# Performance work log

Measured on AMD Instinct MI355X. Metric: run time of the kernel, lower is better.

The kernel has to match this reference:

```python
import jax, jax.numpy as jnp
import numpy as np

H = 1024
E = 8
K = 2
N = 16384
LN_EPS = 1e-5


def _layernorm(h, g, b):
    m = jnp.mean(h, axis=-1, keepdims=True)
    v = jnp.mean(jnp.square(h - m), axis=-1, keepdims=True)
    return (h - m) * jax.lax.rsqrt(v + LN_EPS) * g + b


def setup_inputs() -> dict:
    key = jax.random.key(0)
    ks = jax.random.split(key, 8)
    s = 0.02
    return {
        "x": jax.random.normal(ks[0], (N, H), dtype=jnp.float32),
        "Wg": jax.random.normal(ks[1], (H, E), dtype=jnp.float32) * s,
        "bg": jnp.zeros((E,), dtype=jnp.float32),
        "W1": jax.random.normal(ks[2], (E, H, H), dtype=jnp.float32) * s,
        "b1": jnp.zeros((E, H), dtype=jnp.float32),
        "g1": jnp.ones((E, H), dtype=jnp.float32),
        "be1": jnp.zeros((E, H), dtype=jnp.float32),
        "W2": jax.random.normal(ks[3], (E, H, H), dtype=jnp.float32) * s,
        "b2": jnp.zeros((E, H), dtype=jnp.float32),
        "g2": jnp.ones((E, H), dtype=jnp.float32),
        "be2": jnp.zeros((E, H), dtype=jnp.float32),
    }


def reference(x, Wg, bg, W1, b1, g1, be1, W2, b2, g2, be2):
    # Gating: softmax over experts, top-k, renormalize
    gate_probs = jax.nn.softmax(x @ Wg + bg, axis=1)            # [N, E]
    tk_p, tk_i = jax.lax.top_k(gate_probs, K)                    # [N, K]
    tk_p = tk_p / (jnp.sum(tk_p, axis=1, keepdims=True) + 1e-9)
    # Dense per-expert combine weight (zero where expert not selected)
    w = jnp.sum(tk_p[:, :, None] * jax.nn.one_hot(tk_i, E, dtype=x.dtype), axis=1)  # [N, E]

    # ResidualBlock per expert, computed densely for all tokens (dropout = eval/no-op)
    h = jnp.einsum('nh,eho->eno', x, W1) + b1[:, None, :]        # [E, N, H]
    h = jax.nn.relu(_layernorm(h, g1[:, None, :], be1[:, None, :]))
    h = jnp.einsum('enh,eho->eno', h, W2) + b2[:, None, :]
    h = _layernorm(h, g2[:, None, :], be2[:, None, :])
    y = jax.nn.relu(x[None, :, :] + h)                           # [E, N, H]

    moe_out = jnp.einsum('ne,enh->nh', w, y)                     # [N, H]
    return moe_out, gate_probs
```

## Files before the change

### kernel.cpp

```cpp
#include <hip/hip_runtime.h>
#include <cstdint>
#include <cstddef>

constexpr int H_DIM = 1024;
constexpr int NE    = 8;
constexpr int NT    = 16384;
constexpr int NP    = NT * 2;

typedef __attribute__((ext_vector_type(8))) short          short8;
typedef __attribute__((ext_vector_type(8))) unsigned short ushort8;
typedef __attribute__((ext_vector_type(4))) unsigned short ushort4v;
typedef __attribute__((ext_vector_type(4))) float          f32x4;

__device__ __forceinline__ unsigned short f2bf(float f) {
  union { float f; uint32_t u; } c; c.f = f;
  uint32_t u = c.u;
  u = (u + 0x7fffu + ((u >> 16) & 1u)) >> 16;
  return (unsigned short)u;
}
__device__ __forceinline__ float bf2f(unsigned short h) {
  union { uint32_t u; float f; } c; c.u = ((uint32_t)h) << 16;
  return c.f;
}

__device__ __forceinline__ void gload16(const unsigned short* g, unsigned short* l) {
  __builtin_amdgcn_global_load_lds((const __attribute__((address_space(1))) void*)g,
                                   (__attribute__((address_space(3))) void*)l, 16, 0, 0);
}

__global__ __launch_bounds__(256) void transpose_convert_kernel(
    const float* __restrict__ W1, const float* __restrict__ W2,
    unsigned short* __restrict__ T1, unsigned short* __restrict__ T2)
{
  __shared__ float tile[64][65];
  int zi = blockIdx.z;
  const float* W = (zi < 8) ? W1 : W2;
  unsigned short* T = (zi < 8) ? T1 : T2;
  int e  = zi & 7;
  int o0 = blockIdx.x * 64;
  int h0 = blockIdx.y * 64;
  int c  = threadIdx.x & 63;
  int r0 = (threadIdx.x >> 6) * 16;
  const float* src = W + ((size_t)e * H_DIM + h0) * H_DIM + o0;
#pragma unroll
  for (int i = 0; i < 16; ++i)
    tile[r0 + i][c] = src[(size_t)(r0 + i) * H_DIM + c];
  __syncthreads();
  unsigned short* dst = T + ((size_t)e * H_DIM + o0) * H_DIM + h0;
#pragma unroll
  for (int i = 0; i < 16; ++i)
    dst[(size_t)(r0 + i) * H_DIM + c] = f2bf(tile[c][r0 + i]);
}

__global__ __launch_bounds__(256) void xgate_kernel(
    const float* __restrict__ X, const float* __restrict__ Wg,
    const float* __restrict__ bg, unsigned short* __restrict__ Xb,
    float* __restrict__ gate_out, int* __restrict__ tk_e, float* __restrict__ tk_w)
{
  int wid = threadIdx.x >> 6, lane = threadIdx.x & 63;
  int n = blockIdx.x * 4 + wid;
  const float* xr = X + (size_t)n * H_DIM;

  const float4* xp = (const float4*)(xr + lane * 16);
  float4 f0 = xp[0], f1 = xp[1], f2 = xp[2], f3 = xp[3];
  float v[16] = {f0.x,f0.y,f0.z,f0.w, f1.x,f1.y,f1.z,f1.w,
                 f2.x,f2.y,f2.z,f2.w, f3.x,f3.y,f3.z,f3.w};

  ushort8 u0, u1;
#pragma unroll
  for (int j = 0; j < 8; ++j) { u0[j] = f2bf(v[j]); u1[j] = f2bf(v[8 + j]); }
  ushort8* xb = (ushort8*)(Xb + (size_t)n * H_DIM + lane * 16);
  xb[0] = u0; xb[1] = u1;

  float acc[8];
#pragma unroll
  for (int e = 0; e < 8; ++e) acc[e] = 0.f;
#pragma unroll
  for (int j = 0; j < 16; ++j) {
    int h = lane * 16 + j;
    const float4* wg = (const float4*)(Wg + (size_t)h * 8);
    float4 a = wg[0], b = wg[1];
    float xv = v[j];
    acc[0] += xv * a.x; acc[1] += xv * a.y; acc[2] += xv * a.z; acc[3] += xv * a.w;
    acc[4] += xv * b.x; acc[5] += xv * b.y; acc[6] += xv * b.z; acc[7] += xv * b.w;
  }
#pragma unroll
  for (int m = 1; m < 64; m <<= 1) {
#pragma unroll
    for (int e = 0; e < 8; ++e) acc[e] += __shfl_xor(acc[e], m);
  }
#pragma unroll
  for (int e = 0; e < 8; ++e) acc[e] += bg[e];

  float mx = acc[0];
#pragma unroll
  for (int e = 1; e < 8; ++e) mx = fmaxf(mx, acc[e]);
  float g[8], s = 0.f;
#pragma unroll
  for (int e = 0; e < 8; ++e) { g[e] = __expf(acc[e] - mx); s += g[e]; }
  float inv = 1.f / s;
#pragma unroll
  for (int e = 0; e < 8; ++e) g[e] *= inv;

  int e0 = 0; float b0 = g[0];
#pragma unroll
  for (int e = 1; e < 8; ++e) if (g[e] > b0) { b0 = g[e]; e0 = e; }
  int e1 = -1; float b1v = -1.f;
#pragma unroll
  for (int e = 0; e < 8; ++e) if (e != e0 && g[e] > b1v) { b1v = g[e]; e1 = e; }
  float s2 = b0 + b1v + 1e-9f;

  if (lane == 0) {
    float4* gp = (float4*)(gate_out + (size_t)n * 8);
    gp[0] = make_float4(g[0], g[1], g[2], g[3]);
    gp[1] = make_float4(g[4], g[5], g[6], g[7]);
    tk_e[2 * n] = e0; tk_e[2 * n + 1] = e1;
    tk_w[2 * n] = b0 / s2; tk_w[2 * n + 1] = b1v / s2;
  }
}

__global__ __launch_bounds__(256) void hist_kernel(
    const int* __restrict__ tk_e, int* __restrict__ blockHist)
{
  __shared__ int h[8];
  if (threadIdx.x < 8) h[threadIdx.x] = 0;
  __syncthreads();
  int i0 = blockIdx.x * 512 + threadIdx.x;
  atomicAdd(&h[tk_e[i0]], 1);
  atomicAdd(&h[tk_e[i0 + 256]], 1);
  __syncthreads();
  if (threadIdx.x < 8) blockHist[blockIdx.x * 8 + threadIdx.x] = h[threadIdx.x];
}

__global__ void scan_kernel(const int* __restrict__ blockHist,
                            int* __restrict__ blockBase,
                            int* __restrict__ count, int* __restrict__ offs)
{
  int e = threadIdx.x;
  if (e < 8) {
    int run = 0;
    for (int b = 0; b < 64; ++b) { blockBase[b * 8 + e] = run; run += blockHist[b * 8 + e]; }
    count[e] = run;
  }
  __syncthreads();
  if (threadIdx.x == 0) {
    int o = 0;
    for (int k = 0; k < 8; ++k) { offs[k] = o; o += count[k]; }
  }
  __syncthreads();
  if (e < 8) {
    int o = offs[e];
    for (int b = 0; b < 64; ++b) blockBase[b * 8 + e] += o;
  }
}

__global__ __launch_bounds__(256) void place_kernel(
    const int* __restrict__ tk_e, const int* __restrict__ blockBase,
    int* __restrict__ pairTok, int* __restrict__ pairExp, int* __restrict__ slots)
{
  __shared__ int cur[8];
  if (threadIdx.x < 8) cur[threadIdx.x] = blockBase[blockIdx.x * 8 + threadIdx.x];
  __syncthreads();
#pragma unroll
  for (int j = 0; j < 2; ++j) {
    int i = blockIdx.x * 512 + j * 256 + threadIdx.x;
    int e = tk_e[i];
    int s = atomicAdd(&cur[e], 1);
    pairTok[s] = i >> 1; pairExp[s] = e; slots[i] = s;
  }
}

template<bool GATHER>
__global__ __launch_bounds__(256) void gemm_kernel(
    const unsigned short* __restrict__ Ab,
    const unsigned short* __restrict__ Bt,
    const float* __restrict__ bias,
    const int* __restrict__ pairTok,
    const int* __restrict__ count, const int* __restrict__ offs,
    unsigned short* __restrict__ Out)
{
  __shared__ unsigned short As[128 * 32];
  __shared__ unsigned short Bs[128 * 32];

  const int e  = blockIdx.z;
  const int mt = blockIdx.y;
  const int nt = blockIdx.x;
  const int cnt = count[e];
  if (mt * 128 >= cnt) return;
  const int base = offs[e];
  const int tid = threadIdx.x;
  const int w = tid >> 6, l = tid & 63;

  const int r0 = w * 16 + (l >> 2);
  const int kk = (l & 3) * 8;

  int m0 = mt * 128 + r0;      if (m0 >= cnt) m0 = cnt - 1;
  int m1 = mt * 128 + r0 + 64; if (m1 >= cnt) m1 = cnt - 1;
  size_t arow0, arow1;
  if (GATHER) { arow0 = (size_t)pairTok[base + m0]; arow1 = (size_t)pairTok[base + m1]; }
  else        { arow0 = (size_t)(base + m0);        arow1 = (size_t)(base + m1); }
  const unsigned short* aS0 = Ab + arow0 * H_DIM + kk;
  const unsigned short* aS1 = Ab + arow1 * H_DIM + kk;
  const unsigned short* bS0 = Bt + ((size_t)e * H_DIM + nt * 128 + r0) * H_DIM + kk;
  const unsigned short* bS1 = bS0 + (size_t)64 * H_DIM;
  unsigned short* aD0 = As + w * 512;
  unsigned short* aD1 = As + 2048 + w * 512;
  unsigned short* bD0 = Bs + w * 512;
  unsigned short* bD1 = Bs + 2048 + w * 512;

  const int wr = w >> 1, wc = w & 1;
  const int lr = l & 15, lg = l >> 4;

  f32x4 acc[4][4] = {};

  for (int k0 = 0; k0 < H_DIM; k0 += 32) {
    __syncthreads();
    gload16(aS0 + k0, aD0);
    gload16(aS1 + k0, aD1);
    gload16(bS0 + k0, bD0);
    gload16(bS1 + k0, bD1);
    __syncthreads();

    short8 af[4], bfr[4];
#pragma unroll
    for (int i = 0; i < 4; ++i) {
      af[i]  = *(const short8*)&As[(wr * 64 + i * 16 + lr) * 32 + lg * 8];
      bfr[i] = *(const short8*)&Bs[(wc * 64 + i * 16 + lr) * 32 + lg * 8];
    }
#pragma unroll
    for (int m4 = 0; m4 < 4; ++m4)
#pragma unroll
      for (int n4 = 0; n4 < 4; ++n4)
        acc[m4][n4] = __builtin_amdgcn_mfma_f32_16x16x32_bf16(af[m4], bfr[n4], acc[m4][n4], 0, 0, 0);
  }

#pragma unroll
  for (int n4 = 0; n4 < 4; ++n4) {
    int col = nt * 128 + wc * 64 + n4 * 16 + lr;
    float bv = bias[e * H_DIM + col];
#pragma unroll
    for (int m4 = 0; m4 < 4; ++m4) {
#pragma unroll
      for (int r = 0; r < 4; ++r) {
        int grow = mt * 128 + wr * 64 + m4 * 16 + 4 * lg + r;
        if (grow < cnt)
          Out[(size_t)(base + grow) * H_DIM + col] = f2bf(acc[m4][n4][r] + bv);
      }
    }
  }
}

__global__ __launch_bounds__(256) void ln_relu_kernel(
    unsigned short* __restrict__ buf, const float* __restrict__ gamma,
    const float* __restrict__ beta, const int* __restrict__ pairExp)
{
  int wid = threadIdx.x >> 6, lane = threadIdx.x & 63;
  int row = blockIdx.x * 4 + wid;
  int e = pairExp[row];
  unsigned short* r = buf + (size_t)row * H_DIM;
  ushort8 u0 = ((const ushort8*)r)[lane];
  ushort8 u1 = ((const ushort8*)r)[lane + 64];
  float v[16];
#pragma unroll
  for (int j = 0; j < 8; ++j) { v[j] = bf2f(u0[j]); v[8 + j] = bf2f(u1[j]); }
  float s = 0.f, ss = 0.f;
#pragma unroll
  for (int j = 0; j < 16; ++j) { s += v[j]; ss += v[j] * v[j]; }
#pragma unroll
  for (int m = 1; m < 64; m <<= 1) { s += __shfl_xor(s, m); ss += __shfl_xor(ss, m); }
  float mean = s * (1.f / 1024.f);
  float var  = ss * (1.f / 1024.f) - mean * mean;
  float rs   = rsqrtf(var + 1e-5f);

  int h0 = lane * 8, h1 = 512 + lane * 8;
  const float4* gp0 = (const float4*)(gamma + (size_t)e * H_DIM + h0);
  const float4* bp0 = (const float4*)(beta  + (size_t)e * H_DIM + h0);
  const float4* gp1 = (const float4*)(gamma + (size_t)e * H_DIM + h1);
  const float4* bp1 = (const float4*)(beta  + (size_t)e * H_DIM + h1);
  float4 ga = gp0[0], gb = gp0[1], gc = gp1[0], gd = gp1[1];
  float4 ba = bp0[0], bb = bp0[1], bc = bp1[0], bd = bp1[1];
  float gv[16] = {ga.x,ga.y,ga.z,ga.w, gb.x,gb.y,gb.z,gb.w,
                  gc.x,gc.y,gc.z,gc.w, gd.x,gd.y,gd.z,gd.w};
  float bv[16] = {ba.x,ba.y,ba.z,ba.w, bb.x,bb.y,bb.z,bb.w,
                  bc.x,bc.y,bc.z,bc.w, bd.x,bd.y,bd.z,bd.w};
#pragma unroll
  for (int j = 0; j < 8; ++j) {
    float t0 = fmaxf((v[j]     - mean) * rs * gv[j]     + bv[j],     0.f);
    float t1 = fmaxf((v[8 + j] - mean) * rs * gv[8 + j] + bv[8 + j], 0.f);
    u0[j] = f2bf(t0); u1[j] = f2bf(t1);
  }
  ((ushort8*)r)[lane] = u0; ((ushort8*)r)[lane + 64] = u1;
}

__global__ __launch_bounds__(256) void combine_kernel(
    const unsigned short* __restrict__ buf2, const float* __restrict__ X,
    const float* __restrict__ g2, const float* __restrict__ be2,
    const int* __restrict__ slots, const int* __restrict__ tk_e,
    const float* __restrict__ tk_w, float* __restrict__ out)
{
  int wid = threadIdx.x >> 6, lane = threadIdx.x & 63;
  int n = blockIdx.x * 4 + wid;
  int h0 = lane * 8, h1 = 512 + lane * 8;

  const float4* xp0 = (const float4*)(X + (size_t)n * H_DIM + h0);
  const float4* xp1 = (const float4*)(X + (size_t)n * H_DIM + h1);
  float4 xa = xp0[0], xb = xp0[1], xc = xp1[0], xd = xp1[1];
  float xv[16] = {xa.x,xa.y,xa.z,xa.w, xb.x,xb.y,xb.z,xb.w,
                  xc.x,xc.y,xc.z,xc.w, xd.x,xd.y,xd.z,xd.w};
  float o[16];
#pragma unroll
  for (int j = 0; j < 16; ++j) o[j] = 0.f;

#pragma unroll
  for (int k = 0; k < 2; ++k) {
    int slot = slots[2 * n + k];
    int e = tk_e[2 * n + k];
    float w = tk_w[2 * n + k];
    const unsigned short* r = buf2 + (size_t)slot * H_DIM;
    ushort8 u0 = ((const ushort8*)r)[lane];
    ushort8 u1 = ((const ushort8*)r)[lane + 64];
    float v[16];
#pragma unroll
    for (int j = 0; j < 8; ++j) { v[j] = bf2f(u0[j]); v[8 + j] = bf2f(u1[j]); }
    float s = 0.f, ss = 0.f;
#pragma unroll
    for (int j = 0; j < 16; ++j) { s += v[j]; ss += v[j] * v[j]; }
#pragma unroll
    for (int m = 1; m < 64; m <<= 1) { s += __shfl_xor(s, m); ss += __shfl_xor(ss, m); }
    float mean = s * (1.f / 1024.f);
    float var  = ss * (1.f / 1024.f) - mean * mean;
    float rs   = rsqrtf(var + 1e-5f);

    const float4* gp0 = (const float4*)(g2  + (size_t)e * H_DIM + h0);
    const float4* bp0 = (const float4*)(be2 + (size_t)e * H_DIM + h0);
    const float4* gp1 = (const float4*)(g2  + (size_t)e * H_DIM + h1);
    const float4* bp1 = (const float4*)(be2 + (size_t)e * H_DIM + h1);
    float4 ga = gp0[0], gb = gp0[1], gc = gp1[0], gd = gp1[1];
    float4 ba = bp0[0], bb = bp0[1], bc = bp1[0], bd = bp1[1];
    float gv[16] = {ga.x,ga.y,ga.z,ga.w, gb.x,gb.y,gb.z,gb.w,
                    gc.x,gc.y,gc.z,gc.w, gd.x,gd.y,gd.z,gd.w};
    float bvv[16] = {ba.x,ba.y,ba.z,ba.w, bb.x,bb.y,bb.z,bb.w,
                     bc.x,bc.y,bc.z,bc.w, bd.x,bd.y,bd.z,bd.w};
#pragma unroll
    for (int j = 0; j < 16; ++j) {
      float u = (v[j] - mean) * rs * gv[j] + bvv[j];
      float y = fmaxf(xv[j] + u, 0.f);
      o[j] += w * y;
    }
  }

  float4* op0 = (float4*)(out + (size_t)n * H_DIM + h0);
  float4* op1 = (float4*)(out + (size_t)n * H_DIM + h1);
  op0[0] = make_float4(o[0], o[1], o[2], o[3]);
  op0[1] = make_float4(o[4], o[5], o[6], o[7]);
  op1[0] = make_float4(o[8], o[9], o[10], o[11]);
  op1[1] = make_float4(o[12], o[13], o[14], o[15]);
}

extern "C" void kernel_launch(void* const* d_in, const int* in_sizes, int n_in,
                              void* d_out, int out_size, void* d_ws, size_t ws_size,
                              hipStream_t stream)
{
  const float* x   = (const float*)d_in[0];
  const float* Wg  = (const float*)d_in[1];
  const float* bg  = (const float*)d_in[2];
  const float* W1  = (const float*)d_in[3];
  const float* b1  = (const float*)d_in[4];
  const float* g1  = (const float*)d_in[5];
  const float* be1 = (const float*)d_in[6];
  const float* W2  = (const float*)d_in[7];
  const float* b2  = (const float*)d_in[8];
  const float* g2  = (const float*)d_in[9];
  const float* be2 = (const float*)d_in[10];
  float* out = (float*)d_out;
  float* gate_out = out + (size_t)NT * H_DIM;

  char* ws = (char*)d_ws;
  size_t off = 0;
  auto alloc = [&](size_t bytes) { char* p = ws + off; off += (bytes + 255) & ~(size_t)255; return p; };
  unsigned short* w1bt = (unsigned short*)alloc((size_t)NE * H_DIM * H_DIM * 2);
  unsigned short* w2bt = (unsigned short*)alloc((size_t)NE * H_DIM * H_DIM * 2);
  unsigned short* buf1 = (unsigned short*)alloc((size_t)NP * H_DIM * 2);
  unsigned short* buf2 = (unsigned short*)alloc((size_t)NP * H_DIM * 2);
  int*   tk_e      = (int*)alloc((size_t)NP * 4);
  float* tk_w      = (float*)alloc((size_t)NP * 4);
  int*   pairTok   = (int*)alloc((size_t)NP * 4);
  int*   pairExp   = (int*)alloc((size_t)NP * 4);
  int*   slots     = (int*)alloc((size_t)NP * 4);
  int*   blockHist = (int*)alloc(64 * 8 * 4);
  int*   blockBase = (int*)alloc(64 * 8 * 4);
  int*   count     = (int*)alloc(8 * 4);
  int*   offs      = (int*)alloc(8 * 4);
  (void)in_sizes; (void)n_in; (void)out_size; (void)ws_size;

  unsigned short* Xb = buf2;

  transpose_convert_kernel<<<dim3(16, 16, 16), 256, 0, stream>>>(W1, W2, w1bt, w2bt);
  xgate_kernel<<<dim3(NT / 4), 256, 0, stream>>>(x, Wg, bg, Xb, gate_out, tk_e, tk_w);
  hist_kernel<<<dim3(64), 256, 0, stream>>>(tk_e, blockHist);
  scan_kernel<<<dim3(1), 64, 0, stream>>>(blockHist, blockBase, count, offs);
  place_kernel<<<dim3(64), 256, 0, stream>>>(tk_e, blockBase, pairTok, pairExp, slots);
  gemm_kernel<true><<<dim3(8, 128, 8), 256, 0, stream>>>(
      Xb, w1bt, b1, pairTok, count, offs, buf1);
  ln_relu_kernel<<<dim3(NP / 4), 256, 0, stream>>>(buf1, g1, be1, pairExp);
  gemm_kernel<false><<<dim3(8, 128, 8), 256, 0, stream>>>(
      buf1, w2bt, b2, pairTok, count, offs, buf2);
  combine_kernel<<<dim3(NT / 4), 256, 0, stream>>>(
      buf2, x, g2, be2, slots, tk_e, tk_w, out);
}
```

Measured before the change: 423.9 us.

## Rewrite grouped expert GEMM with 256x256 tiles, double-buffering, and compact worklist

The grouped expert GEMM moves from 128x128x32 tiles with 4 waves to 256x256x64 tiles with 8 waves. LDS is double-buffered with an XOR swizzle, and the next tiles are prefetched asynchronously while MFMAs run, with raised priority around the MFMA block. A new worklist kernel builds a compact list of the non-empty (expert, n-tile, m-tile) tiles, and blocks are remapped across the XCDs so empty tiles are not launched and neighbouring tiles share cache. The aim is more data reuse per load, overlap of load latency with compute, and less launch waste, at the cost of larger LDS and register use plus one extra tiny kernel.

```diff
diff --git a/kernel.cpp b/kernel.cpp
--- a/kernel.cpp
+++ b/kernel.cpp
@@ -7,9 +7,12 @@
 constexpr int NT    = 16384;
 constexpr int NP    = NT * 2;
 
+constexpr int BM = 256, BN = 256, BK = 64;
+constexpr int NKT = H_DIM / BK;
+constexpr int MAX_WG = NE * (NT / BM) * (H_DIM / BN);
+
 typedef __attribute__((ext_vector_type(8))) short          short8;
 typedef __attribute__((ext_vector_type(8))) unsigned short ushort8;
-typedef __attribute__((ext_vector_type(4))) unsigned short ushort4v;
 typedef __attribute__((ext_vector_type(4))) float          f32x4;
 
 __device__ __forceinline__ unsigned short f2bf(float f) {
@@ -170,84 +173,182 @@
   }
 }
 
+__global__ void worklist_kernel(const int* __restrict__ count,
+                                int* __restrict__ wl, int* __restrict__ wlCount)
+{
+  __shared__ int nmt[8], ebase[8], totalS;
+  if (threadIdx.x == 0) {
+    int o = 0;
+    for (int e = 0; e < 8; ++e) {
+      nmt[e] = (count[e] + BM - 1) / BM;
+      ebase[e] = o;
+      o += nmt[e] * (H_DIM / BN);
+    }
+    totalS = o;
+    wlCount[0] = o;
+  }
+  __syncthreads();
+  int total = totalS;
+  for (int i = threadIdx.x; i < total; i += blockDim.x) {
+    int e = 0;
+    while (e < 7 && i >= ebase[e + 1]) ++e;
+    int loc = i - ebase[e];
+    int nt = loc / nmt[e];
+    int mt = loc - nt * nmt[e];
+    wl[i] = (e << 20) | (nt << 16) | mt;
+  }
+}
+
 template<bool GATHER>
-__global__ __launch_bounds__(256) void gemm_kernel(
+__global__ __launch_bounds__(512, 2) void gemm8_kernel(
     const unsigned short* __restrict__ Ab,
     const unsigned short* __restrict__ Bt,
     const float* __restrict__ bias,
     const int* __restrict__ pairTok,
     const int* __restrict__ count, const int* __restrict__ offs,
+    const int* __restrict__ wl, const int* __restrict__ wlCount,
     unsigned short* __restrict__ Out)
 {
-  __shared__ unsigned short As[128 * 32];
-  __shared__ unsigned short Bs[128 * 32];
-
-  const int e  = blockIdx.z;
-  const int mt = blockIdx.y;
-  const int nt = blockIdx.x;
-  const int cnt = count[e];
-  if (mt * 128 >= cnt) return;
-  const int base = offs[e];
+  __shared__ unsigned short As[2 * 2 * 8192];
+  __shared__ unsigned short Bs[2 * 2 * 8192];
+
+  const int total = wlCount[0];
+  const int orig = blockIdx.x;
+  if (orig >= total) return;
+  const int qq = total >> 3, rr = total & 7;
+  const int xcd = orig & 7, sub = orig >> 3;
+  const int idx = (xcd < rr ? xcd * (qq + 1) : rr * (qq + 1) + (xcd - rr) * qq) + sub;
+  const int ent = wl[idx];
+  const int e = ent >> 20, ntb = (ent >> 16) & 15, mtb = ent & 0xffff;
+  const int cnt = count[e], base = offs[e];
+
   const int tid = threadIdx.x;
-  const int w = tid >> 6, l = tid & 63;
-
-  const int r0 = w * 16 + (l >> 2);
-  const int kk = (l & 3) * 8;
-
-  int m0 = mt * 128 + r0;      if (m0 >= cnt) m0 = cnt - 1;
-  int m1 = mt * 128 + r0 + 64; if (m1 >= cnt) m1 = cnt - 1;
-  size_t arow0, arow1;
-  if (GATHER) { arow0 = (size_t)pairTok[base + m0]; arow1 = (size_t)pairTok[base + m1]; }
-  else        { arow0 = (size_t)(base + m0);        arow1 = (size_t)(base + m1); }
-  const unsigned short* aS0 = Ab + arow0 * H_DIM + kk;
-  const unsigned short* aS1 = Ab + arow1 * H_DIM + kk;
-  const unsigned short* bS0 = Bt + ((size_t)e * H_DIM + nt * 128 + r0) * H_DIM + kk;
-  const unsigned short* bS1 = bS0 + (size_t)64 * H_DIM;
-  unsigned short* aD0 = As + w * 512;
-  unsigned short* aD1 = As + 2048 + w * 512;
-  unsigned short* bD0 = Bs + w * 512;
-  unsigned short* bD1 = Bs + 2048 + w * 512;
-
-  const int wr = w >> 1, wc = w & 1;
-  const int lr = l & 15, lg = l >> 4;
-
-  f32x4 acc[4][4] = {};
-
-  for (int k0 = 0; k0 < H_DIM; k0 += 32) {
-    __syncthreads();
-    gload16(aS0 + k0, aD0);
-    gload16(aS1 + k0, aD1);
-    gload16(bS0 + k0, bD0);
-    gload16(bS1 + k0, bD1);
-    __syncthreads();
-
-    short8 af[4], bfr[4];
-#pragma unroll
-    for (int i = 0; i < 4; ++i) {
-      af[i]  = *(const short8*)&As[(wr * 64 + i * 16 + lr) * 32 + lg * 8];
-      bfr[i] = *(const short8*)&Bs[(wc * 64 + i * 16 + lr) * 32 + lg * 8];
+  const int wid = tid >> 6, l = tid & 63;
+  const int wr = wid >> 2, wc = wid & 3;
+
+  const int rih0 = (((tid >> 6)) >> 1) * 16 + ((tid >> 2) & 15);
+  const int rih1 = ((8 + (tid >> 6)) >> 1) * 16 + ((tid >> 2) & 15);
+  const int selem = ((tid >> 6) & 1) * 32 + (((tid & 3) * 8) ^ (((tid >> 5) & 1) << 4));
+
+  const unsigned short* ap[4];
+  const unsigned short* bp[4];
+  {
+    int g0 = mtb * 256 + rih0;       if (g0 >= cnt) g0 = cnt - 1;
+    int g1 = mtb * 256 + rih1;       if (g1 >= cnt) g1 = cnt - 1;
+    int g2 = mtb * 256 + 128 + rih0; if (g2 >= cnt) g2 = cnt - 1;
+    int g3 = mtb * 256 + 128 + rih1; if (g3 >= cnt) g3 = cnt - 1;
+    size_t r0, r1, r2, r3;
+    if (GATHER) {
+      r0 = (size_t)pairTok[base + g0]; r1 = (size_t)pairTok[base + g1];
+      r2 = (size_t)pairTok[base + g2]; r3 = (size_t)pairTok[base + g3];
+    } else {
+      r0 = (size_t)(base + g0); r1 = (size_t)(base + g1);
+      r2 = (size_t)(base + g2); r3 = (size_t)(base + g3);
     }
-#pragma unroll
-    for (int m4 = 0; m4 < 4; ++m4)
-#pragma unroll
-      for (int n4 = 0; n4 < 4; ++n4)
-        acc[m4][n4] = __builtin_amdgcn_mfma_f32_16x16x32_bf16(af[m4], bfr[n4], acc[m4][n4], 0, 0, 0);
-  }
-
-#pragma unroll
-  for (int n4 = 0; n4 < 4; ++n4) {
-    int col = nt * 128 + wc * 64 + n4 * 16 + lr;
-    float bv = bias[e * H_DIM + col];
-#pragma unroll
-    for (int m4 = 0; m4 < 4; ++m4) {
-#pragma unroll
-      for (int r = 0; r < 4; ++r) {
-        int grow = mt * 128 + wr * 64 + m4 * 16 + 4 * lg + r;
-        if (grow < cnt)
-          Out[(size_t)(base + grow) * H_DIM + col] = f2bf(acc[m4][n4][r] + bv);
-      }
+    ap[0] = Ab + r0 * H_DIM + selem;
+    ap[1] = Ab + r1 * H_DIM + selem;
+    ap[2] = Ab + r2 * H_DIM + selem;
+    ap[3] = Ab + r3 * H_DIM + selem;
+    const unsigned short* bbase = Bt + ((size_t)e * H_DIM + ntb * 256) * H_DIM + selem;
+    bp[0] = bbase + (size_t)(rih0)       * H_DIM;
+    bp[1] = bbase + (size_t)(rih1)       * H_DIM;
+    bp[2] = bbase + (size_t)(128 + rih0) * H_DIM;
+    bp[3] = bbase + (size_t)(128 + rih1) * H_DIM;
+  }
+
+#define A_DST(t, h, i) (As + ((t) & 1) * 16384 + (h) * 8192 + (i) * 4096 + wid * 512)
+#define B_DST(t, h, i) (Bs + ((t) & 1) * 16384 + (h) * 8192 + (i) * 4096 + wid * 512)
+
+  const int loff = ((l & 15) * 64 + (l >> 4) * 16) ^ (((l >> 3) & 1) << 5);
+  const char* AsB = (const char*)As + wr * 16384 + loff;
+  const char* BsB = (const char*)Bs + (wc >> 1) * 16384 + loff;
+  const int bsub = (wc & 1) * 4;
+
+  gload16(ap[0], A_DST(0, 0, 0)); gload16(ap[1], A_DST(0, 0, 1));
+  gload16(ap[2], A_DST(0, 1, 0)); gload16(ap[3], A_DST(0, 1, 1));
+  gload16(bp[0], B_DST(0, 0, 0)); gload16(bp[1], B_DST(0, 0, 1));
+  gload16(bp[2], B_DST(0, 1, 0)); gload16(bp[3], B_DST(0, 1, 1));
+  gload16(bp[0] + BK, B_DST(1, 0, 0)); gload16(bp[1] + BK, B_DST(1, 0, 1));
+  gload16(bp[2] + BK, B_DST(1, 1, 0)); gload16(bp[3] + BK, B_DST(1, 1, 1));
+  asm volatile("s_waitcnt vmcnt(4)" ::: "memory");
+  __builtin_amdgcn_s_barrier();
+
+  f32x4 acc[8][4] = {};
+
+  for (int t = 0; t < NKT; ++t) {
+    const int db = t & 1;
+    const int dboff = db * 32768;
+    short8 bfrag[4][2];
+#pragma unroll
+    for (int q = 0; q < 4; ++q) {
+      short8 af[2][2];
+#pragma unroll
+      for (int j = 0; j < 2; ++j)
+#pragma unroll
+        for (int ks = 0; ks < 2; ++ks)
+          af[j][ks] = *(const short8*)(AsB + dboff + ((q * 2 + j) * 2 + ks) * 1024);
+      if (q == 0) {
+#pragma unroll
+        for (int r = 0; r < 4; ++r)
+#pragma unroll
+          for (int ks = 0; ks < 2; ++ks)
+            bfrag[r][ks] = *(const short8*)(BsB + dboff + ((bsub + r) * 2 + ks) * 1024);
+      }
+      if (q == 0 && t + 1 < NKT) {
+        gload16(ap[0] + (t + 1) * BK, A_DST(t + 1, 0, 0));
+        gload16(ap[1] + (t + 1) * BK, A_DST(t + 1, 0, 1));
+      }
+      if (q == 1 && t + 1 < NKT) {
+        gload16(ap[2] + (t + 1) * BK, A_DST(t + 1, 1, 0));
+        gload16(ap[3] + (t + 1) * BK, A_DST(t + 1, 1, 1));
+      }
+      if (q == 2 && t + 2 < NKT) {
+        gload16(bp[0] + (t + 2) * BK, B_DST(t + 2, 0, 0));
+        gload16(bp[1] + (t + 2) * BK, B_DST(t + 2, 0, 1));
+      }
+      if (q == 3 && t + 2 < NKT) {
+        gload16(bp[2] + (t + 2) * BK, B_DST(t + 2, 1, 0));
+        gload16(bp[3] + (t + 2) * BK, B_DST(t + 2, 1, 1));
+      }
+      __builtin_amdgcn_s_barrier();
+      __builtin_amdgcn_s_setprio(1);
+#pragma unroll
+      for (int j = 0; j < 2; ++j)
+#pragma unroll
+        for (int r = 0; r < 4; ++r)
+#pragma unroll
+          for (int ks = 0; ks < 2; ++ks)
+            acc[q * 2 + j][r] = __builtin_amdgcn_mfma_f32_16x16x32_bf16(
+                af[j][ks], bfrag[r][ks], acc[q * 2 + j][r], 0, 0, 0);
+      __builtin_amdgcn_s_setprio(0);
+      if (q == 3) {
+        if (t + 2 < NKT) asm volatile("s_waitcnt vmcnt(4)" ::: "memory");
+        else             asm volatile("s_waitcnt vmcnt(0)" ::: "memory");
+      }
+      __builtin_amdgcn_s_barrier();
     }
   }
+
+  float bvv[4];
+#pragma unroll
+  for (int r = 0; r < 4; ++r)
+    bvv[r] = bias[e * H_DIM + ntb * 256 + wc * 64 + r * 16 + (l & 15)];
+#pragma unroll
+  for (int j = 0; j < 8; ++j) {
+    int grow0 = mtb * 256 + wr * 128 + j * 16 + (l >> 4) * 4;
+#pragma unroll
+    for (int r = 0; r < 4; ++r) {
+      int gcol = ntb * 256 + wc * 64 + r * 16 + (l & 15);
+#pragma unroll
+      for (int v = 0; v < 4; ++v) {
+        int row = grow0 + v;
+        if (row < cnt)
+          Out[(size_t)(base + row) * H_DIM + gcol] = f2bf(acc[j][r][v] + bvv[r]);
+      }
+    }
+  }
+#undef A_DST
+#undef B_DST
 }
 
 __global__ __launch_bounds__(256) void ln_relu_kernel(
@@ -391,6 +492,8 @@
   int*   blockBase = (int*)alloc(64 * 8 * 4);
   int*   count     = (int*)alloc(8 * 4);
   int*   offs      = (int*)alloc(8 * 4);
+  int*   wl        = (int*)alloc(MAX_WG * 4);
+  int*   wlCount   = (int*)alloc(4);
   (void)in_sizes; (void)n_in; (void)out_size; (void)ws_size;
 
   unsigned short* Xb = buf2;
@@ -399,12 +502,13 @@
   xgate_kernel<<<dim3(NT / 4), 256, 0, stream>>>(x, Wg, bg, Xb, gate_out, tk_e, tk_w);
   hist_kernel<<<dim3(64), 256, 0, stream>>>(tk_e, blockHist);
   scan_kernel<<<dim3(1), 64, 0, stream>>>(blockHist, blockBase, count, offs);
+  worklist_kernel<<<dim3(1), 256, 0, stream>>>(count, wl, wlCount);
   place_kernel<<<dim3(64), 256, 0, stream>>>(tk_e, blockBase, pairTok, pairExp, slots);
-  gemm_kernel<true><<<dim3(8, 128, 8), 256, 0, stream>>>(
-      Xb, w1bt, b1, pairTok, count, offs, buf1);
+  gemm8_kernel<true><<<dim3(MAX_WG), 512, 0, stream>>>(
+      Xb, w1bt, b1, pairTok, count, offs, wl, wlCount, buf1);
   ln_relu_kernel<<<dim3(NP / 4), 256, 0, stream>>>(buf1, g1, be1, pairExp);
-  gemm_kernel<false><<<dim3(8, 128, 8), 256, 0, stream>>>(
-      buf1, w2bt, b2, pairTok, count, offs, buf2);
+  gemm8_kernel<false><<<dim3(MAX_WG), 512, 0, stream>>>(
+      buf1, w2bt, b2, pairTok, count, offs, wl, wlCount, buf2);
   combine_kernel<<<dim3(NT / 4), 256, 0, stream>>>(
       buf2, x, g2, be2, slots, tk_e, tk_w, out);
 }
```

Result: faster. 413.4 us (-2.5%).

## Replace expert GEMM with 256x256 double-buffered 8-phase pipelined kernel over compact worklist

Applied to the files above, without the earlier changes.

Swaps the 128x128, K=32 single-buffered expert GEMM for a 512-thread kernel that computes 256x256 tiles with K=64. It double-buffers swizzled LDS tiles and interleaves global-to-LDS loads with MFMA phases, using explicit barriers, waitcnts and setprio. The scan kernel now also builds a compact worklist of the non-empty expert tiles, and the work-item index is remapped so consecutive items land on the same XCD. The aim is more data reuse per byte loaded, hidden memory latency and fewer idle blocks. In exchange it uses 128KB of LDS per block, which limits occupancy to one block per CU, and the hand-written synchronisation is fragile.

```diff
diff --git a/kernel.cpp b/kernel.cpp
--- a/kernel.cpp
+++ b/kernel.cpp
@@ -7,9 +7,12 @@
 constexpr int NT    = 16384;
 constexpr int NP    = NT * 2;
 
+constexpr int GBM = 256, GBN = 256, GBK = 64;
+constexpr int GNKT = H_DIM / GBK;
+constexpr int MAX_WG = (NP / GBM + NE) * (H_DIM / GBN);
+
 typedef __attribute__((ext_vector_type(8))) short          short8;
 typedef __attribute__((ext_vector_type(8))) unsigned short ushort8;
-typedef __attribute__((ext_vector_type(4))) unsigned short ushort4v;
 typedef __attribute__((ext_vector_type(4))) float          f32x4;
 
 __device__ __forceinline__ unsigned short f2bf(float f) {
@@ -132,10 +135,12 @@
   if (threadIdx.x < 8) blockHist[blockIdx.x * 8 + threadIdx.x] = h[threadIdx.x];
 }
 
-__global__ void scan_kernel(const int* __restrict__ blockHist,
-                            int* __restrict__ blockBase,
-                            int* __restrict__ count, int* __restrict__ offs)
-{
+__global__ void scan_worklist_kernel(const int* __restrict__ blockHist,
+                                     int* __restrict__ blockBase,
+                                     int* __restrict__ count, int* __restrict__ offs,
+                                     int* __restrict__ wl, int* __restrict__ wlCount)
+{
+  __shared__ int nmt[8], ebase[8], totalS;
   int e = threadIdx.x;
   if (e < 8) {
     int run = 0;
@@ -144,13 +149,27 @@
   }
   __syncthreads();
   if (threadIdx.x == 0) {
-    int o = 0;
-    for (int k = 0; k < 8; ++k) { offs[k] = o; o += count[k]; }
+    int o = 0, wo = 0;
+    for (int k = 0; k < 8; ++k) {
+      offs[k] = o; o += count[k];
+      nmt[k] = (count[k] + GBM - 1) / GBM;
+      ebase[k] = wo; wo += nmt[k] * (H_DIM / GBN);
+    }
+    totalS = wo; wlCount[0] = wo;
   }
   __syncthreads();
   if (e < 8) {
     int o = offs[e];
     for (int b = 0; b < 64; ++b) blockBase[b * 8 + e] += o;
+  }
+  int total = totalS;
+  for (int i = threadIdx.x; i < total; i += blockDim.x) {
+    int ee = 0;
+    while (ee < 7 && i >= ebase[ee + 1]) ++ee;
+    int loc = i - ebase[ee];
+    int nt = loc / nmt[ee];
+    int mt = loc - nt * nmt[ee];
+    wl[i] = (ee << 20) | (nt << 16) | mt;
   }
 }
 
@@ -171,83 +190,161 @@
 }
 
 template<bool GATHER>
-__global__ __launch_bounds__(256) void gemm_kernel(
+__global__ __launch_bounds__(512, 2) void gemm8p_kernel(
     const unsigned short* __restrict__ Ab,
     const unsigned short* __restrict__ Bt,
     const float* __restrict__ bias,
     const int* __restrict__ pairTok,
     const int* __restrict__ count, const int* __restrict__ offs,
+    const int* __restrict__ wl, const int* __restrict__ wlCount,
     unsigned short* __restrict__ Out)
 {
-  __shared__ unsigned short As[128 * 32];
-  __shared__ unsigned short Bs[128 * 32];
-
-  const int e  = blockIdx.z;
-  const int mt = blockIdx.y;
-  const int nt = blockIdx.x;
-  const int cnt = count[e];
-  if (mt * 128 >= cnt) return;
-  const int base = offs[e];
+  __shared__ unsigned short lds[65536];
+
+  const int total = wlCount[0];
+  const int orig = blockIdx.x;
+  if (orig >= total) return;
+  const int qq = total >> 3, rr = total & 7;
+  const int xcd = orig & 7, sub = orig >> 3;
+  const int idx = (xcd < rr ? xcd * (qq + 1) : rr * (qq + 1) + (xcd - rr) * qq) + sub;
+  const int ent = wl[idx];
+  const int e = ent >> 20, ntb = (ent >> 16) & 15, mtb = ent & 0xffff;
+  const int cnt = count[e], base = offs[e];
+
   const int tid = threadIdx.x;
-  const int w = tid >> 6, l = tid & 63;
-
-  const int r0 = w * 16 + (l >> 2);
-  const int kk = (l & 3) * 8;
-
-  int m0 = mt * 128 + r0;      if (m0 >= cnt) m0 = cnt - 1;
-  int m1 = mt * 128 + r0 + 64; if (m1 >= cnt) m1 = cnt - 1;
-  size_t arow0, arow1;
-  if (GATHER) { arow0 = (size_t)pairTok[base + m0]; arow1 = (size_t)pairTok[base + m1]; }
-  else        { arow0 = (size_t)(base + m0);        arow1 = (size_t)(base + m1); }
-  const unsigned short* aS0 = Ab + arow0 * H_DIM + kk;
-  const unsigned short* aS1 = Ab + arow1 * H_DIM + kk;
-  const unsigned short* bS0 = Bt + ((size_t)e * H_DIM + nt * 128 + r0) * H_DIM + kk;
-  const unsigned short* bS1 = bS0 + (size_t)64 * H_DIM;
-  unsigned short* aD0 = As + w * 512;
-  unsigned short* aD1 = As + 2048 + w * 512;
-  unsigned short* bD0 = Bs + w * 512;
-  unsigned short* bD1 = Bs + 2048 + w * 512;
-
-  const int wr = w >> 1, wc = w & 1;
-  const int lr = l & 15, lg = l >> 4;
-
-  f32x4 acc[4][4] = {};
-
-  for (int k0 = 0; k0 < H_DIM; k0 += 32) {
-    __syncthreads();
-    gload16(aS0 + k0, aD0);
-    gload16(aS1 + k0, aD1);
-    gload16(bS0 + k0, bD0);
-    gload16(bS1 + k0, bD1);
-    __syncthreads();
-
-    short8 af[4], bfr[4];
-#pragma unroll
-    for (int i = 0; i < 4; ++i) {
-      af[i]  = *(const short8*)&As[(wr * 64 + i * 16 + lr) * 32 + lg * 8];
-      bfr[i] = *(const short8*)&Bs[(wc * 64 + i * 16 + lr) * 32 + lg * 8];
+  const int wid = tid >> 6, l = tid & 63;
+  const int wr = wid >> 2, wc = wid & 3;
+
+  const int rwh  = (wid >> 1) * 16 + (l >> 2);
+  const int ksl  = wid & 1;
+  const int koff = ksl * 32 + (((l & 3) * 8) ^ (((l >> 5) & 1) << 4));
+
+  const unsigned short* aptr[2][2];
+  const unsigned short* bptr[2][2];
+#pragma unroll
+  for (int ha = 0; ha < 2; ++ha)
+#pragma unroll
+    for (int j = 0; j < 2; ++j) {
+      int grow = mtb * GBM + ha * 128 + j * 64 + rwh;
+      if (grow >= cnt) grow = cnt - 1;
+      size_t arow = GATHER ? (size_t)pairTok[base + grow] : (size_t)(base + grow);
+      aptr[ha][j] = Ab + arow * H_DIM + koff;
+      int col = ntb * GBN + ha * 128 + j * 64 + rwh;
+      bptr[ha][j] = Bt + ((size_t)e * H_DIM + col) * H_DIM + koff;
     }
-#pragma unroll
-    for (int m4 = 0; m4 < 4; ++m4)
-#pragma unroll
-      for (int n4 = 0; n4 < 4; ++n4)
-        acc[m4][n4] = __builtin_amdgcn_mfma_f32_16x16x32_bf16(af[m4], bfr[n4], acc[m4][n4], 0, 0, 0);
-  }
-
-#pragma unroll
-  for (int n4 = 0; n4 < 4; ++n4) {
-    int col = nt * 128 + wc * 64 + n4 * 16 + lr;
-    float bv = bias[e * H_DIM + col];
-#pragma unroll
-    for (int m4 = 0; m4 < 4; ++m4) {
-#pragma unroll
-      for (int r = 0; r < 4; ++r) {
-        int grow = mt * 128 + wr * 64 + m4 * 16 + 4 * lg + r;
-        if (grow < cnt)
-          Out[(size_t)(base + grow) * H_DIM + col] = f2bf(acc[m4][n4][r] + bv);
+
+  char* ldsb = (char*)lds;
+  const char* ldsc = (const char*)lds;
+  const int loff = ((l & 15) * 64 + (l >> 4) * 16) ^ (((l >> 3) & 1) << 5);
+  const int dsub = ((wid >> 1) * 2 + ksl) * 1024;
+
+#define STAGE_A(t, ha) do { \
+    char* _d = ldsb + ((t) & 1) * 32768 + (ha) * 16384 + dsub; \
+    gload16(aptr[ha][0] + (size_t)(t) * GBK, (unsigned short*)_d); \
+    gload16(aptr[ha][1] + (size_t)(t) * GBK, (unsigned short*)(_d + 8192)); \
+  } while (0)
+#define STAGE_B(t, hb) do { \
+    char* _d = ldsb + 65536 + ((t) & 1) * 32768 + (hb) * 16384 + dsub; \
+    gload16(bptr[hb][0] + (size_t)(t) * GBK, (unsigned short*)_d); \
+    gload16(bptr[hb][1] + (size_t)(t) * GBK, (unsigned short*)(_d + 8192)); \
+  } while (0)
+
+  short8 af[4][2], bf0[2][2], bf1[2][2];
+  f32x4 acc[2][2][4][2] = {};
+
+#define LOAD_A(b, ha) do { \
+  _Pragma("unroll") for (int f = 0; f < 4; ++f) \
+  _Pragma("unroll") for (int ks = 0; ks < 2; ++ks) \
+    af[f][ks] = *(const short8*)(ldsc + (b) * 32768 + (ha) * 16384 + ((wr * 4 + f) * 2 + ks) * 1024 + loff); \
+  } while (0)
+#define LOAD_B(b, hb, B) do { \
+  _Pragma("unroll") for (int g = 0; g < 2; ++g) \
+  _Pragma("unroll") for (int ks = 0; ks < 2; ++ks) \
+    B[g][ks] = *(const short8*)(ldsc + 65536 + (b) * 32768 + (hb) * 16384 + ((wc * 2 + g) * 2 + ks) * 1024 + loff); \
+  } while (0)
+#define MFMA_PH(rq, ch, B) do { \
+  __builtin_amdgcn_s_setprio(1); \
+  _Pragma("unroll") for (int f = 0; f < 4; ++f) \
+  _Pragma("unroll") for (int g = 0; g < 2; ++g) \
+  _Pragma("unroll") for (int ks = 0; ks < 2; ++ks) \
+    acc[rq][ch][f][g] = __builtin_amdgcn_mfma_f32_16x16x32_bf16(af[f][ks], B[g][ks], acc[rq][ch][f][g], 0, 0, 0); \
+  __builtin_amdgcn_s_setprio(0); \
+  } while (0)
+#define PH_SYNC do { \
+    __builtin_amdgcn_s_barrier(); \
+    asm volatile("s_waitcnt lgkmcnt(0)" ::: "memory"); \
+    __builtin_amdgcn_sched_barrier(0); \
+  } while (0)
+
+  STAGE_A(0, 0); STAGE_B(0, 0); STAGE_A(0, 1); STAGE_B(0, 1);
+  STAGE_A(1, 0); STAGE_B(1, 0);
+  asm volatile("s_waitcnt vmcnt(4)" ::: "memory");
+  __builtin_amdgcn_s_barrier();
+
+#pragma unroll 1
+  for (int i = 0; i < GNKT / 2; ++i) {
+    const int t1 = 2 * i + 1, T = 2 * i + 2, U = 2 * i + 3;
+    LOAD_A(0, 0); LOAD_B(0, 0, bf0);
+    STAGE_A(t1, 1);
+    PH_SYNC; MFMA_PH(0, 0, bf0);
+    __builtin_amdgcn_s_barrier();
+    LOAD_B(0, 1, bf1);
+    STAGE_B(t1, 1);
+    PH_SYNC; MFMA_PH(0, 1, bf1);
+    __builtin_amdgcn_s_barrier();
+    LOAD_A(0, 1);
+    if (T < GNKT) STAGE_A(T, 0);
+    PH_SYNC; MFMA_PH(1, 0, bf0);
+    __builtin_amdgcn_s_barrier();
+    if (T < GNKT) STAGE_B(T, 0);
+    PH_SYNC; MFMA_PH(1, 1, bf1);
+    if (i == GNKT / 2 - 1) asm volatile("s_waitcnt vmcnt(0)" ::: "memory");
+    else                   asm volatile("s_waitcnt vmcnt(4)" ::: "memory");
+    __builtin_amdgcn_s_barrier();
+    LOAD_A(1, 0); LOAD_B(1, 0, bf0);
+    if (T < GNKT) STAGE_A(T, 1);
+    PH_SYNC; MFMA_PH(0, 0, bf0);
+    __builtin_amdgcn_s_barrier();
+    LOAD_B(1, 1, bf1);
+    if (T < GNKT) STAGE_B(T, 1);
+    PH_SYNC; MFMA_PH(0, 1, bf1);
+    __builtin_amdgcn_s_barrier();
+    LOAD_A(1, 1);
+    if (U < GNKT) STAGE_A(U, 0);
+    PH_SYNC; MFMA_PH(1, 0, bf0);
+    __builtin_amdgcn_s_barrier();
+    if (U < GNKT) STAGE_B(U, 0);
+    PH_SYNC; MFMA_PH(1, 1, bf1);
+    if (i < GNKT / 2 - 1) asm volatile("s_waitcnt vmcnt(4)" ::: "memory");
+    __builtin_amdgcn_s_barrier();
+  }
+
+#undef STAGE_A
+#undef STAGE_B
+#undef LOAD_A
+#undef LOAD_B
+#undef MFMA_PH
+#undef PH_SYNC
+
+#pragma unroll
+  for (int rq = 0; rq < 2; ++rq)
+#pragma unroll
+    for (int ch = 0; ch < 2; ++ch)
+#pragma unroll
+      for (int g = 0; g < 2; ++g) {
+        int col = ntb * GBN + ch * 128 + wc * 32 + g * 16 + (l & 15);
+        float bv = bias[e * H_DIM + col];
+#pragma unroll
+        for (int f = 0; f < 4; ++f) {
+          int row0 = mtb * GBM + rq * 128 + wr * 64 + f * 16 + (l >> 4) * 4;
+#pragma unroll
+          for (int v = 0; v < 4; ++v) {
+            int row = row0 + v;
+            if (row < cnt)
+              Out[(size_t)(base + row) * H_DIM + col] = f2bf(acc[rq][ch][f][g][v] + bv);
+          }
+        }
       }
-    }
-  }
 }
 
 __global__ __launch_bounds__(256) void ln_relu_kernel(
@@ -391,6 +488,8 @@
   int*   blockBase = (int*)alloc(64 * 8 * 4);
   int*   count     = (int*)alloc(8 * 4);
   int*   offs      = (int*)alloc(8 * 4);
+  int*   wl        = (int*)alloc(MAX_WG * 4);
+  int*   wlCount   = (int*)alloc(4);
   (void)in_sizes; (void)n_in; (void)out_size; (void)ws_size;
 
   unsigned short* Xb = buf2;
@@ -398,13 +497,13 @@
   transpose_convert_kernel<<<dim3(16, 16, 16), 256, 0, stream>>>(W1, W2, w1bt, w2bt);
   xgate_kernel<<<dim3(NT / 4), 256, 0, stream>>>(x, Wg, bg, Xb, gate_out, tk_e, tk_w);
   hist_kernel<<<dim3(64), 256, 0, stream>>>(tk_e, blockHist);
-  scan_kernel<<<dim3(1), 64, 0, stream>>>(blockHist, blockBase, count, offs);
+  scan_worklist_kernel<<<dim3(1), 256, 0, stream>>>(blockHist, blockBase, count, offs, wl, wlCount);
   place_kernel<<<dim3(64), 256, 0, stream>>>(tk_e, blockBase, pairTok, pairExp, slots);
-  gemm_kernel<true><<<dim3(8, 128, 8), 256, 0, stream>>>(
-      Xb, w1bt, b1, pairTok, count, offs, buf1);
+  gemm8p_kernel<true><<<dim3(MAX_WG), 512, 0, stream>>>(
+      Xb, w1bt, b1, pairTok, count, offs, wl, wlCount, buf1);
   ln_relu_kernel<<<dim3(NP / 4), 256, 0, stream>>>(buf1, g1, be1, pairExp);
-  gemm_kernel<false><<<dim3(8, 128, 8), 256, 0, stream>>>(
-      buf1, w2bt, b2, pairTok, count, offs, buf2);
+  gemm8p_kernel<false><<<dim3(MAX_WG), 512, 0, stream>>>(
+      buf1, w2bt, b2, pairTok, count, offs, wl, wlCount, buf2);
   combine_kernel<<<dim3(NT / 4), 256, 0, stream>>>(
       buf2, x, g2, be2, slots, tk_e, tk_w, out);
 }
```

Measured after the change: 418.7 us. Within noise of the previous version (-1.2%).
